# Kernel tuning notes

Measured on AMD Instinct MI355X. Metric: run time of the kernel, lower is better.

The kernel has to match this reference:

```python
import jax, jax.numpy as jnp
import numpy as np

B, C, H, W = 8, 96, 512, 96  # W == w_size (required by the view semantics)
EPS = 1e-5


def setup_inputs() -> dict:
    key = jax.random.key(0)
    ks = jax.random.split(key, 3)
    x = jax.random.normal(ks[0], (B, C, H, W), dtype=jnp.float32)
    bn_gamma = jnp.ones((C,), jnp.float32)
    bn_beta = jnp.zeros((C,), jnp.float32)
    bn_mean = jnp.zeros((C,), jnp.float32)   # BatchNorm running mean (eval mode)
    bn_var = jnp.ones((C,), jnp.float32)     # BatchNorm running var  (eval mode)
    qkv_w = jax.random.normal(ks[1], (3 * C, C), jnp.float32) * (1.0 / np.sqrt(C))
    qkv_b = jnp.zeros((3 * C,), jnp.float32)
    return {"x": x, "bn_gamma": bn_gamma, "bn_beta": bn_beta,
            "bn_mean": bn_mean, "bn_var": bn_var,
            "qkv_w": qkv_w, "qkv_b": qkv_b}


def reference(x, bn_gamma, bn_beta, bn_mean, bn_var, qkv_w, qkv_b):
    # BatchNorm2d (eval-mode affine normalize), fused scale/shift per channel
    inv = (bn_gamma / jnp.sqrt(bn_var + EPS))[:, None, None]
    xn = (x - bn_mean[:, None, None]) * inv + bn_beta[:, None, None]
    # 1x1 conv QKV projection: [b,c,h,w] -> [b,3c,h,w]
    qkv = jnp.einsum('bchw,oc->bohw', xn, qkv_w) + qkv_b[None, :, None, None]
    q, k, v = jnp.split(qkv, 3, axis=1)  # each [b,c,h,w]
    # per-row attention over the width axis (w == w_size)
    qp = jnp.transpose(q, (0, 2, 3, 1))  # [b,h,w,c]
    kp = jnp.transpose(k, (0, 2, 3, 1))  # [b,h,w,c]
    vp = jnp.transpose(v, (0, 2, 3, 1))  # [b,h,w,c]
    score = jnp.einsum('bhqc,bhkc->bhqk', qp, kp)  # [b,h,w,w]
    attn = jax.nn.softmax(score, axis=-1)
    xt = jnp.einsum('bhqk,bhkc->bhqc', attn, vp)   # [b,h,w,c]
    out = jnp.transpose(xt, (0, 3, 1, 2)) + x       # residual add, [b,c,h,w]
    return out
```

## Files before the change

kernel.cpp:

```cpp
#include <hip/hip_runtime.h>

#define C_ 96
#define H_ 512
#define W_ 96
#define HW_ 49152
#define CHW_ 4718592
#define PIT 104
#define REG 9984

typedef _Float16 f16x8 __attribute__((ext_vector_type(8)));
typedef _Float16 f16x4 __attribute__((ext_vector_type(4)));
typedef float    f32x4 __attribute__((ext_vector_type(4)));

__global__ void prep_kernel(const float* __restrict__ wq,
                            const float* __restrict__ gamma,
                            const float* __restrict__ beta,
                            const float* __restrict__ mean,
                            const float* __restrict__ var,
                            _Float16* __restrict__ whf,
                            float* __restrict__ inv,
                            float* __restrict__ shift)
{
    int i = blockIdx.x * 256 + threadIdx.x;
    if (i < 3 * C_ * C_) whf[i] = (_Float16)wq[i];
    if (i < C_) {
        float iv = gamma[i] * rsqrtf(var[i] + 1e-5f);
        inv[i]   = iv;
        shift[i] = beta[i] - mean[i] * iv;
    }
}

__global__ __launch_bounds__(384, 3) void attn_kernel(
    const float* __restrict__ x,
    const _Float16* __restrict__ wqkv,
    const float* __restrict__ bias,
    const float* __restrict__ bninv,
    const float* __restrict__ bnshift,
    float* __restrict__ out)
{
    __shared__ _Float16 smem[3 * REG];
    _Float16* XNV = smem;
    _Float16* QP  = smem + REG;
    _Float16* Ks  = smem + 2 * REG;

    const int tid  = threadIdx.x;
    const int ws   = tid >> 6;
    const int lane = tid & 63;
    const int q4   = lane >> 4;
    const int n16  = lane & 15;

    const int bh = blockIdx.x;
    const size_t base = (size_t)(bh >> 9) * CHW_ + (size_t)(bh & 511) * W_;
    const int w0 = 16 * ws + 4 * q4;

    f32x4 xr[6];
    #pragma unroll
    for (int t = 0; t < 6; ++t) {
        const int c = 16 * t + n16;
        xr[t] = *(const f32x4*)(x + base + (size_t)c * HW_ + w0);
        const float iv = bninv[c], sh = bnshift[c];
        #pragma unroll
        for (int r = 0; r < 4; ++r)
            XNV[(w0 + r) * PIT + c] = (_Float16)(xr[t][r] * iv + sh);
    }
    __syncthreads();

    const int obase = 48 * ws;
    f32x4 acc[3][6];
    #pragma unroll
    for (int mt = 0; mt < 3; ++mt) {
        const f32x4 bb = *(const f32x4*)(bias + obase + 16 * mt + 4 * q4);
        #pragma unroll
        for (int nt = 0; nt < 6; ++nt) acc[mt][nt] = bb;
    }
    #pragma unroll
    for (int kk = 0; kk < 3; ++kk) {
        f16x8 bfr[6];
        #pragma unroll
        for (int nt = 0; nt < 6; ++nt)
            bfr[nt] = *(const f16x8*)(XNV + (16 * nt + n16) * PIT + 32 * kk + 8 * q4);
        #pragma unroll
        for (int mt = 0; mt < 3; ++mt) {
            const f16x8 afr = *(const f16x8*)(wqkv + (obase + 16 * mt + n16) * 96 + 32 * kk + 8 * q4);
            #pragma unroll
            for (int nt = 0; nt < 6; ++nt)
                acc[mt][nt] = __builtin_amdgcn_mfma_f32_16x16x32_f16(afr, bfr[nt], acc[mt][nt], 0, 0, 0);
        }
    }
    __syncthreads();

    #pragma unroll
    for (int mt = 0; mt < 3; ++mt) {
        const int o = obase + 16 * mt + 4 * q4;
        #pragma unroll
        for (int nt = 0; nt < 6; ++nt) {
            const int w = 16 * nt + n16;
            if (obase < 96) {
                f16x4 pk;
                #pragma unroll
                for (int r = 0; r < 4; ++r) pk[r] = (_Float16)acc[mt][nt][r];
                *(f16x4*)(QP + w * PIT + o) = pk;
            } else if (obase < 192) {
                f16x4 pk;
                #pragma unroll
                for (int r = 0; r < 4; ++r) pk[r] = (_Float16)acc[mt][nt][r];
                *(f16x4*)(Ks + w * PIT + (o - 96)) = pk;
            } else {
                #pragma unroll
                for (int r = 0; r < 4; ++r)
                    XNV[(o - 192 + r) * PIT + w] = (_Float16)acc[mt][nt][r];
            }
        }
    }
    __syncthreads();

    f32x4 sacc[6];
    #pragma unroll
    for (int nt = 0; nt < 6; ++nt) sacc[nt] = f32x4{0.f, 0.f, 0.f, 0.f};
    #pragma unroll
    for (int kk = 0; kk < 3; ++kk) {
        const f16x8 qa = *(const f16x8*)(QP + (16 * ws + n16) * PIT + 32 * kk + 8 * q4);
        #pragma unroll
        for (int nt = 0; nt < 6; ++nt) {
            const f16x8 kb = *(const f16x8*)(Ks + (16 * nt + n16) * PIT + 32 * kk + 8 * q4);
            sacc[nt] = __builtin_amdgcn_mfma_f32_16x16x32_f16(qa, kb, sacc[nt], 0, 0, 0);
        }
    }

    float invl[4];
    #pragma unroll
    for (int r = 0; r < 4; ++r) {
        float m = sacc[0][r];
        #pragma unroll
        for (int nt = 1; nt < 6; ++nt) m = fmaxf(m, sacc[nt][r]);
        #pragma unroll
        for (int d = 1; d < 16; d <<= 1) m = fmaxf(m, __shfl_xor(m, d, 64));
        float s = 0.f;
        #pragma unroll
        for (int nt = 0; nt < 6; ++nt) {
            const float e = __expf(sacc[nt][r] - m);
            sacc[nt][r] = e;
            s += e;
        }
        #pragma unroll
        for (int d = 1; d < 16; d <<= 1) s += __shfl_xor(s, d, 64);
        invl[r] = 1.f / s;
    }
    #pragma unroll
    for (int nt = 0; nt < 6; ++nt) {
        #pragma unroll
        for (int r = 0; r < 4; ++r)
            QP[(16 * ws + 4 * q4 + r) * PIT + 16 * nt + n16] = (_Float16)sacc[nt][r];
    }

    f32x4 oacc[6];
    #pragma unroll
    for (int nt = 0; nt < 6; ++nt) oacc[nt] = f32x4{0.f, 0.f, 0.f, 0.f};
    #pragma unroll
    for (int kk = 0; kk < 3; ++kk) {
        const f16x8 pa = *(const f16x8*)(QP + (16 * ws + n16) * PIT + 32 * kk + 8 * q4);
        #pragma unroll
        for (int nt = 0; nt < 6; ++nt) {
            const f16x8 vb = *(const f16x8*)(XNV + (16 * nt + n16) * PIT + 32 * kk + 8 * q4);
            oacc[nt] = __builtin_amdgcn_mfma_f32_16x16x32_f16(pa, vb, oacc[nt], 0, 0, 0);
        }
    }

    #pragma unroll
    for (int nt = 0; nt < 6; ++nt) {
        const int c = 16 * nt + n16;
        f32x4 o4;
        #pragma unroll
        for (int r = 0; r < 4; ++r)
            o4[r] = oacc[nt][r] * invl[r] + xr[nt][r];
        *(f32x4*)(out + base + (size_t)c * HW_ + w0) = o4;
    }
}

extern "C" void kernel_launch(void* const* d_in, const int* in_sizes, int n_in,
                              void* d_out, int out_size, void* d_ws, size_t ws_size,
                              hipStream_t stream)
{
    const float* x     = (const float*)d_in[0];
    const float* gamma = (const float*)d_in[1];
    const float* beta  = (const float*)d_in[2];
    const float* mean  = (const float*)d_in[3];
    const float* var   = (const float*)d_in[4];
    const float* qkvw  = (const float*)d_in[5];
    const float* qkvb  = (const float*)d_in[6];
    float* out = (float*)d_out;

    _Float16* whf = (_Float16*)d_ws;
    float*  inv  = (float*)((char*)d_ws + 55296);
    float*  shf  = (float*)((char*)d_ws + 55296 + 384);

    prep_kernel<<<108, 256, 0, stream>>>(qkvw, gamma, beta, mean, var, whf, inv, shf);
    attn_kernel<<<4096, 384, 0, stream>>>(x, whf, qkvb, inv, shf, out);
}
```

Before: 341.3 us.

## Persistent 8-row blocks with prefetch, BN folded into weights, double-buffered LDS

Each block now handles 8 consecutive h-rows in a loop, launching 512 blocks instead of 4096. The x loads for the next row are prefetched into registers and written to a second LDS buffer to overlap global latency with compute. BatchNorm is folded into the fp16 QKV weights and a precomputed bias in the prep kernel, so the per-element normalize disappears. The V projection is recomputed in a transposed orientation, the softmax normalization is applied before the PV matmul, and barriers are replaced with a waitcnt plus s_barrier. The costs are fewer blocks in flight, larger LDS per block, and fp16 rounding of unnormalized x combined with weights scaled by the BN factor.

```diff
diff --git a/kernel.cpp b/kernel.cpp
--- a/kernel.cpp
+++ b/kernel.cpp
@@ -12,168 +12,237 @@
 typedef _Float16 f16x4 __attribute__((ext_vector_type(4)));
 typedef float    f32x4 __attribute__((ext_vector_type(4)));
 
+#define MFMA16 __builtin_amdgcn_mfma_f32_16x16x32_f16
+
+#define BAR() do { asm volatile("s_waitcnt lgkmcnt(0)" ::: "memory"); \
+                   __builtin_amdgcn_s_barrier(); } while (0)
+
 __global__ void prep_kernel(const float* __restrict__ wq,
                             const float* __restrict__ gamma,
                             const float* __restrict__ beta,
                             const float* __restrict__ mean,
                             const float* __restrict__ var,
+                            const float* __restrict__ qkvb,
                             _Float16* __restrict__ whf,
-                            float* __restrict__ inv,
-                            float* __restrict__ shift)
+                            float* __restrict__ bprime)
 {
     int i = blockIdx.x * 256 + threadIdx.x;
-    if (i < 3 * C_ * C_) whf[i] = (_Float16)wq[i];
-    if (i < C_) {
-        float iv = gamma[i] * rsqrtf(var[i] + 1e-5f);
-        inv[i]   = iv;
-        shift[i] = beta[i] - mean[i] * iv;
+    if (i < 3 * C_ * C_) {
+        int c = i % C_;
+        float iv = gamma[c] * rsqrtf(var[c] + 1e-5f);
+        whf[i] = (_Float16)(wq[i] * iv);
+    }
+    if (i < 3 * C_) {
+        float acc = qkvb[i];
+        for (int c = 0; c < C_; ++c) {
+            float iv = gamma[c] * rsqrtf(var[c] + 1e-5f);
+            acc += wq[i * C_ + c] * (beta[c] - mean[c] * iv);
+        }
+        bprime[i] = acc;
     }
 }
 
 __global__ __launch_bounds__(384, 3) void attn_kernel(
     const float* __restrict__ x,
     const _Float16* __restrict__ wqkv,
-    const float* __restrict__ bias,
-    const float* __restrict__ bninv,
-    const float* __restrict__ bnshift,
+    const float* __restrict__ bprime,
     float* __restrict__ out)
 {
-    __shared__ _Float16 smem[3 * REG];
-    _Float16* XNV = smem;
-    _Float16* QP  = smem + REG;
-    _Float16* Ks  = smem + 2 * REG;
+    __shared__ __align__(16) _Float16 smem[4 * REG];
 
     const int tid  = threadIdx.x;
     const int ws   = tid >> 6;
     const int lane = tid & 63;
     const int q4   = lane >> 4;
     const int n16  = lane & 15;
-
-    const int bh = blockIdx.x;
-    const size_t base = (size_t)(bh >> 9) * CHW_ + (size_t)(bh & 511) * W_;
-    const int w0 = 16 * ws + 4 * q4;
-
-    f32x4 xr[6];
+    const int w0   = 16 * ws + 4 * q4;
+
+    _Float16* Rcur = smem;
+    _Float16* Rnxt = smem + REG;
+    _Float16* QP   = smem + 2 * REG;
+    _Float16* Ks   = smem + 3 * REG;
+
+    size_t base = (size_t)(blockIdx.x >> 6) * CHW_
+                + (size_t)((blockIdx.x & 63) * 8) * W_;
+
+    f32x4 xr[6], xrn[6];
+
     #pragma unroll
-    for (int t = 0; t < 6; ++t) {
-        const int c = 16 * t + n16;
-        xr[t] = *(const f32x4*)(x + base + (size_t)c * HW_ + w0);
-        const float iv = bninv[c], sh = bnshift[c];
+    for (int t6 = 0; t6 < 6; ++t6)
+        xr[t6] = *(const f32x4*)(x + base + (size_t)(16 * t6 + n16) * HW_ + w0);
+    #pragma unroll
+    for (int t6 = 0; t6 < 6; ++t6) {
+        const int c = 16 * t6 + n16;
         #pragma unroll
         for (int r = 0; r < 4; ++r)
-            XNV[(w0 + r) * PIT + c] = (_Float16)(xr[t][r] * iv + sh);
-    }
-    __syncthreads();
+            Rcur[(w0 + r) * PIT + c] = (_Float16)xr[t6][r];
+    }
+    BAR();
 
     const int obase = 48 * ws;
-    f32x4 acc[3][6];
-    #pragma unroll
-    for (int mt = 0; mt < 3; ++mt) {
-        const f32x4 bb = *(const f32x4*)(bias + obase + 16 * mt + 4 * q4);
-        #pragma unroll
-        for (int nt = 0; nt < 6; ++nt) acc[mt][nt] = bb;
-    }
-    #pragma unroll
-    for (int kk = 0; kk < 3; ++kk) {
-        f16x8 bfr[6];
-        #pragma unroll
-        for (int nt = 0; nt < 6; ++nt)
-            bfr[nt] = *(const f16x8*)(XNV + (16 * nt + n16) * PIT + 32 * kk + 8 * q4);
-        #pragma unroll
-        for (int mt = 0; mt < 3; ++mt) {
-            const f16x8 afr = *(const f16x8*)(wqkv + (obase + 16 * mt + n16) * 96 + 32 * kk + 8 * q4);
-            #pragma unroll
-            for (int nt = 0; nt < 6; ++nt)
-                acc[mt][nt] = __builtin_amdgcn_mfma_f32_16x16x32_f16(afr, bfr[nt], acc[mt][nt], 0, 0, 0);
-        }
-    }
-    __syncthreads();
-
-    #pragma unroll
-    for (int mt = 0; mt < 3; ++mt) {
-        const int o = obase + 16 * mt + 4 * q4;
+    const int ob    = 192 + 48 * (ws - 4);
+
+    #pragma unroll 1
+    for (int t = 0; t < 8; ++t) {
+        if (t < 7) {
+            #pragma unroll
+            for (int t6 = 0; t6 < 6; ++t6)
+                xrn[t6] = *(const f32x4*)(x + base + W_
+                              + (size_t)(16 * t6 + n16) * HW_ + w0);
+        }
+
+        f32x4 acc[18];
+        if (ws < 4) {
+            #pragma unroll
+            for (int mt = 0; mt < 3; ++mt) {
+                const f32x4 bb = *(const f32x4*)(bprime + obase + 16 * mt + 4 * q4);
+                #pragma unroll
+                for (int nt = 0; nt < 6; ++nt) acc[6 * mt + nt] = bb;
+            }
+            #pragma unroll
+            for (int kk = 0; kk < 3; ++kk) {
+                f16x8 bfr[6];
+                #pragma unroll
+                for (int nt = 0; nt < 6; ++nt)
+                    bfr[nt] = *(const f16x8*)(Rcur + (16 * nt + n16) * PIT + 32 * kk + 8 * q4);
+                #pragma unroll
+                for (int mt = 0; mt < 3; ++mt) {
+                    const f16x8 afr = *(const f16x8*)(wqkv + (obase + 16 * mt + n16) * 96 + 32 * kk + 8 * q4);
+                    #pragma unroll
+                    for (int nt = 0; nt < 6; ++nt)
+                        acc[6 * mt + nt] = MFMA16(afr, bfr[nt], acc[6 * mt + nt], 0, 0, 0);
+                }
+            }
+        } else {
+            #pragma unroll
+            for (int ot = 0; ot < 3; ++ot) {
+                const float bv = bprime[ob + 16 * ot + n16];
+                #pragma unroll
+                for (int wt = 0; wt < 6; ++wt) acc[3 * wt + ot] = f32x4{bv, bv, bv, bv};
+            }
+            #pragma unroll
+            for (int kk = 0; kk < 3; ++kk) {
+                f16x8 xa[6];
+                #pragma unroll
+                for (int wt = 0; wt < 6; ++wt)
+                    xa[wt] = *(const f16x8*)(Rcur + (16 * wt + n16) * PIT + 32 * kk + 8 * q4);
+                #pragma unroll
+                for (int ot = 0; ot < 3; ++ot) {
+                    const f16x8 wb = *(const f16x8*)(wqkv + (ob + 16 * ot + n16) * 96 + 32 * kk + 8 * q4);
+                    #pragma unroll
+                    for (int wt = 0; wt < 6; ++wt)
+                        acc[3 * wt + ot] = MFMA16(xa[wt], wb, acc[3 * wt + ot], 0, 0, 0);
+                }
+            }
+        }
+        BAR();
+
+        if (ws < 4) {
+            #pragma unroll
+            for (int mt = 0; mt < 3; ++mt) {
+                const int o = obase + 16 * mt + 4 * q4;
+                #pragma unroll
+                for (int nt = 0; nt < 6; ++nt) {
+                    f16x4 pk;
+                    #pragma unroll
+                    for (int r = 0; r < 4; ++r) pk[r] = (_Float16)acc[6 * mt + nt][r];
+                    const int w = 16 * nt + n16;
+                    if (obase < 96) *(f16x4*)(QP + w * PIT + o) = pk;
+                    else            *(f16x4*)(Ks + w * PIT + (o - 96)) = pk;
+                }
+            }
+        } else {
+            #pragma unroll
+            for (int ot = 0; ot < 3; ++ot) {
+                const int c = ob - 192 + 16 * ot + n16;
+                #pragma unroll
+                for (int wt = 0; wt < 6; ++wt) {
+                    f16x4 pk;
+                    #pragma unroll
+                    for (int r = 0; r < 4; ++r) pk[r] = (_Float16)acc[3 * wt + ot][r];
+                    *(f16x4*)(Rcur + c * PIT + 16 * wt + 4 * q4) = pk;
+                }
+            }
+        }
+        BAR();
+
+        f32x4 sacc[6];
+        #pragma unroll
+        for (int nt = 0; nt < 6; ++nt) sacc[nt] = f32x4{0.f, 0.f, 0.f, 0.f};
+        #pragma unroll
+        for (int kk = 0; kk < 3; ++kk) {
+            const f16x8 qb = *(const f16x8*)(QP + (16 * ws + n16) * PIT + 32 * kk + 8 * q4);
+            #pragma unroll
+            for (int nt = 0; nt < 6; ++nt) {
+                const f16x8 ka = *(const f16x8*)(Ks + (16 * nt + n16) * PIT + 32 * kk + 8 * q4);
+                sacc[nt] = MFMA16(ka, qb, sacc[nt], 0, 0, 0);
+            }
+        }
+        float mr0 = sacc[0][0], mr1 = sacc[0][1], mr2 = sacc[0][2], mr3 = sacc[0][3];
+        #pragma unroll
+        for (int nt = 1; nt < 6; ++nt) {
+            mr0 = fmaxf(mr0, sacc[nt][0]); mr1 = fmaxf(mr1, sacc[nt][1]);
+            mr2 = fmaxf(mr2, sacc[nt][2]); mr3 = fmaxf(mr3, sacc[nt][3]);
+        }
+        float m = fmaxf(fmaxf(mr0, mr1), fmaxf(mr2, mr3));
+        m = fmaxf(m, __shfl_xor(m, 16));
+        m = fmaxf(m, __shfl_xor(m, 32));
+        float sr0 = 0.f, sr1 = 0.f, sr2 = 0.f, sr3 = 0.f;
         #pragma unroll
         for (int nt = 0; nt < 6; ++nt) {
-            const int w = 16 * nt + n16;
-            if (obase < 96) {
-                f16x4 pk;
-                #pragma unroll
-                for (int r = 0; r < 4; ++r) pk[r] = (_Float16)acc[mt][nt][r];
-                *(f16x4*)(QP + w * PIT + o) = pk;
-            } else if (obase < 192) {
-                f16x4 pk;
-                #pragma unroll
-                for (int r = 0; r < 4; ++r) pk[r] = (_Float16)acc[mt][nt][r];
-                *(f16x4*)(Ks + w * PIT + (o - 96)) = pk;
-            } else {
+            sacc[nt][0] = __expf(sacc[nt][0] - m); sr0 += sacc[nt][0];
+            sacc[nt][1] = __expf(sacc[nt][1] - m); sr1 += sacc[nt][1];
+            sacc[nt][2] = __expf(sacc[nt][2] - m); sr2 += sacc[nt][2];
+            sacc[nt][3] = __expf(sacc[nt][3] - m); sr3 += sacc[nt][3];
+        }
+        float s = (sr0 + sr1) + (sr2 + sr3);
+        s += __shfl_xor(s, 16);
+        s += __shfl_xor(s, 32);
+        const float pinv = 1.0f / s;
+        #pragma unroll
+        for (int nt = 0; nt < 6; ++nt) {
+            f16x4 pk;
+            #pragma unroll
+            for (int r = 0; r < 4; ++r) pk[r] = (_Float16)(sacc[nt][r] * pinv);
+            *(f16x4*)(QP + (16 * ws + n16) * PIT + 16 * nt + 4 * q4) = pk;
+        }
+
+        f32x4 oacc[6];
+        #pragma unroll
+        for (int nt = 0; nt < 6; ++nt) oacc[nt] = f32x4{0.f, 0.f, 0.f, 0.f};
+        #pragma unroll
+        for (int kk = 0; kk < 3; ++kk) {
+            const f16x8 pa = *(const f16x8*)(QP + (16 * ws + n16) * PIT + 32 * kk + 8 * q4);
+            #pragma unroll
+            for (int nt = 0; nt < 6; ++nt) {
+                const f16x8 vb = *(const f16x8*)(Rcur + (16 * nt + n16) * PIT + 32 * kk + 8 * q4);
+                oacc[nt] = MFMA16(pa, vb, oacc[nt], 0, 0, 0);
+            }
+        }
+
+        if (t < 7) {
+            #pragma unroll
+            for (int t6 = 0; t6 < 6; ++t6) {
+                const int c = 16 * t6 + n16;
                 #pragma unroll
                 for (int r = 0; r < 4; ++r)
-                    XNV[(o - 192 + r) * PIT + w] = (_Float16)acc[mt][nt][r];
-            }
-        }
-    }
-    __syncthreads();
-
-    f32x4 sacc[6];
-    #pragma unroll
-    for (int nt = 0; nt < 6; ++nt) sacc[nt] = f32x4{0.f, 0.f, 0.f, 0.f};
-    #pragma unroll
-    for (int kk = 0; kk < 3; ++kk) {
-        const f16x8 qa = *(const f16x8*)(QP + (16 * ws + n16) * PIT + 32 * kk + 8 * q4);
+                    Rnxt[(w0 + r) * PIT + c] = (_Float16)xrn[t6][r];
+            }
+        }
+
         #pragma unroll
         for (int nt = 0; nt < 6; ++nt) {
-            const f16x8 kb = *(const f16x8*)(Ks + (16 * nt + n16) * PIT + 32 * kk + 8 * q4);
-            sacc[nt] = __builtin_amdgcn_mfma_f32_16x16x32_f16(qa, kb, sacc[nt], 0, 0, 0);
-        }
-    }
-
-    float invl[4];
-    #pragma unroll
-    for (int r = 0; r < 4; ++r) {
-        float m = sacc[0][r];
-        #pragma unroll
-        for (int nt = 1; nt < 6; ++nt) m = fmaxf(m, sacc[nt][r]);
-        #pragma unroll
-        for (int d = 1; d < 16; d <<= 1) m = fmaxf(m, __shfl_xor(m, d, 64));
-        float s = 0.f;
-        #pragma unroll
-        for (int nt = 0; nt < 6; ++nt) {
-            const float e = __expf(sacc[nt][r] - m);
-            sacc[nt][r] = e;
-            s += e;
-        }
-        #pragma unroll
-        for (int d = 1; d < 16; d <<= 1) s += __shfl_xor(s, d, 64);
-        invl[r] = 1.f / s;
-    }
-    #pragma unroll
-    for (int nt = 0; nt < 6; ++nt) {
-        #pragma unroll
-        for (int r = 0; r < 4; ++r)
-            QP[(16 * ws + 4 * q4 + r) * PIT + 16 * nt + n16] = (_Float16)sacc[nt][r];
-    }
-
-    f32x4 oacc[6];
-    #pragma unroll
-    for (int nt = 0; nt < 6; ++nt) oacc[nt] = f32x4{0.f, 0.f, 0.f, 0.f};
-    #pragma unroll
-    for (int kk = 0; kk < 3; ++kk) {
-        const f16x8 pa = *(const f16x8*)(QP + (16 * ws + n16) * PIT + 32 * kk + 8 * q4);
-        #pragma unroll
-        for (int nt = 0; nt < 6; ++nt) {
-            const f16x8 vb = *(const f16x8*)(XNV + (16 * nt + n16) * PIT + 32 * kk + 8 * q4);
-            oacc[nt] = __builtin_amdgcn_mfma_f32_16x16x32_f16(pa, vb, oacc[nt], 0, 0, 0);
-        }
-    }
-
-    #pragma unroll
-    for (int nt = 0; nt < 6; ++nt) {
-        const int c = 16 * nt + n16;
-        f32x4 o4;
-        #pragma unroll
-        for (int r = 0; r < 4; ++r)
-            o4[r] = oacc[nt][r] * invl[r] + xr[nt][r];
-        *(f32x4*)(out + base + (size_t)c * HW_ + w0) = o4;
+            f32x4 o4;
+            #pragma unroll
+            for (int r = 0; r < 4; ++r) o4[r] = oacc[nt][r] + xr[nt][r];
+            *(f32x4*)(out + base + (size_t)(16 * nt + n16) * HW_ + w0) = o4;
+        }
+
+        #pragma unroll
+        for (int t6 = 0; t6 < 6; ++t6) xr[t6] = xrn[t6];
+        base += W_;
+        { _Float16* tmp = Rcur; Rcur = Rnxt; Rnxt = tmp; }
+        BAR();
     }
 }
 
@@ -190,10 +259,9 @@
     const float* qkvb  = (const float*)d_in[6];
     float* out = (float*)d_out;
 
-    _Float16* whf = (_Float16*)d_ws;
-    float*  inv  = (float*)((char*)d_ws + 55296);
-    float*  shf  = (float*)((char*)d_ws + 55296 + 384);
-
-    prep_kernel<<<108, 256, 0, stream>>>(qkvw, gamma, beta, mean, var, whf, inv, shf);
-    attn_kernel<<<4096, 384, 0, stream>>>(x, whf, qkvb, inv, shf, out);
+    _Float16* whf    = (_Float16*)d_ws;
+    float*    bprime = (float*)((char*)d_ws + 55296);
+
+    prep_kernel<<<108, 256, 0, stream>>>(qkvw, gamma, beta, mean, var, qkvb, whf, bprime);
+    attn_kernel<<<512, 384, 0, stream>>>(x, whf, bprime, out);
 }
```

New measurement: 431.4 us. 1.26x slower.
